# Performance work log

Measured on AMD Instinct MI355X. Metric: run time of the kernel, lower is better.

Reference implementation:

```python
import jax, jax.numpy as jnp
import numpy as np


def lstm_cell(x, h, c, Wih, Whh, bih, bhh):
    # PyTorch LSTM gate order: i, f, g, o
    gates = x @ Wih.T + h @ Whh.T + bih + bhh
    i, f, g, o = jnp.split(gates, 4, axis=-1)
    c_new = jax.nn.sigmoid(f) * c + jax.nn.sigmoid(i) * jnp.tanh(g)
    h_new = jax.nn.sigmoid(o) * jnp.tanh(c_new)
    return h_new, c_new


def setup_inputs() -> dict:
    V, E, H, L, S, B, T = 100000, 256, 256, 2, 256, 16, 128
    G = 4 * H
    s = 0.1  # weight scale to keep activations/gradients well-conditioned
    key = jax.random.key(0)
    ks = jax.random.split(key, 16)
    return {
        'source': jax.random.randint(ks[0], (S, B), 0, V),
        'target_size': T,
        'target_embeddings': jax.random.normal(ks[1], (T, 1, E), dtype=jnp.float32),
        'h0': jax.random.normal(ks[2], (L, B, H), dtype=jnp.float32) * s,
        'c0': jax.random.normal(ks[3], (L, B, H), dtype=jnp.float32) * s,
        'embed_table': jax.random.normal(ks[4], (V, E), dtype=jnp.float32) * s,
        'enc_Wih': jax.random.normal(ks[5], (L, G, E), dtype=jnp.float32) * s,
        'enc_Whh': jax.random.normal(ks[6], (L, G, H), dtype=jnp.float32) * s,
        'enc_bih': jax.random.normal(ks[7], (L, G), dtype=jnp.float32) * s,
        'enc_bhh': jax.random.normal(ks[8], (L, G), dtype=jnp.float32) * s,
        'dec_Wih': jax.random.normal(ks[9], (L, G, E), dtype=jnp.float32) * s,
        'dec_Whh': jax.random.normal(ks[10], (L, G, H), dtype=jnp.float32) * s,
        'dec_bih': jax.random.normal(ks[11], (L, G), dtype=jnp.float32) * s,
        'dec_bhh': jax.random.normal(ks[12], (L, G), dtype=jnp.float32) * s,
        'attn_W': jax.random.normal(ks[13], (1, 2 * H), dtype=jnp.float32) * s,
        'attn_b': jnp.zeros((1,), dtype=jnp.float32),
        'comb_W': jax.random.normal(ks[14], (H, 2 * H), dtype=jnp.float32) * s,
        'comb_b': jnp.zeros((H,), dtype=jnp.float32),
    }


def reference(source, target_size, target_embeddings, h0, c0, embed_table,
              enc_Wih, enc_Whh, enc_bih, enc_bhh,
              dec_Wih, dec_Whh, dec_bih, dec_bhh,
              attn_W, attn_b, comb_W, comb_b):
    L = h0.shape[0]
    B = source.shape[1]

    # ---------------- encoder (per-step LSTM loop -> layer-wise scans) ----
    x = embed_table[source]  # [S, B, E]  (dropout is identity at eval)
    h_fin = []
    for l in range(L):
        def step(carry, xt, l=l):
            h, c = carry
            h, c = lstm_cell(xt, h, c, enc_Wih[l], enc_Whh[l], enc_bih[l], enc_bhh[l])
            return (h, c), h
        (hL, cL), x = jax.lax.scan(step, (h0[l], c0[l]), x)
        h_fin.append(hL)
    hidden_final = jnp.stack(h_fin)   # [L, B, H] == hiddens[-1] in the source
    enc_outputs = x                   # [S, B, H] last-layer hidden per step
    S = enc_outputs.shape[0]

    # NOTE (faithful to source bugs): seq2seq sets both decoder hidden AND
    # cell from encoder_hidden[-1], and the decoder runs its LSTM on the raw
    # input `embedding`, discarding the attention-combined output.
    x0 = jnp.tile(target_embeddings[0, 0], (B, 1))  # [B, E]

    def dec_step(carry, _):
        x, h, c = carry
        # per-step Bahdanau-style attention: computed but UNUSED, as in source
        cat = jnp.concatenate([jnp.broadcast_to(x, (S,) + x.shape), enc_outputs], axis=-1)
        w = jax.nn.softmax(cat @ attn_W.T + attn_b, axis=0)       # [S, B, 1]
        applied = (w * enc_outputs).sum(0)                         # [B, H]
        _combined = jax.nn.relu(jnp.concatenate([x, applied], axis=-1) @ comb_W.T + comb_b)
        # actual recurrence: multi-layer LSTM on the raw input x
        inp = x
        hs, cs = [], []
        for l in range(h.shape[0]):
            hl, cl = lstm_cell(inp, h[l], c[l], dec_Wih[l], dec_Whh[l], dec_bih[l], dec_bhh[l])
            hs.append(hl)
            cs.append(cl)
            inp = hl
        return (inp, jnp.stack(hs), jnp.stack(cs)), inp

    _, ys = jax.lax.scan(dec_step, (x0, hidden_final, hidden_final), None,
                         length=target_size - 1)  # ys: [T-1, B, H]
    H = ys.shape[-1]
    preds = jnp.zeros((target_size, 1, B, H), ys.dtype)
    preds = preds.at[1:].set(ys[:, None])  # predictions[0] stays zero
    return preds
```

## Files before the change

kernel.cpp:

```cpp
#include <hip/hip_runtime.h>
#include <hip/hip_bf16.h>

typedef __attribute__((ext_vector_type(8))) short short8;
typedef __attribute__((ext_vector_type(4))) float f32x4;

#define SEQ   256
#define BB    16
#define EE    256
#define HH    256
#define GG    1024
#define TT    128
#define NWG   32
#define KP    264
#define SLOT_S 8192
#define SENT  0xFF80FF80u
#define MAXTRY (1 << 20)

__device__ __forceinline__ float sigm(float x) { return 1.0f / (1.0f + __expf(-x)); }
__device__ __forceinline__ float tanh_f(float x) {
    float e = __expf(2.0f * x);
    return 1.0f - 2.0f / (e + 1.0f);
}
__device__ __forceinline__ void split2s(float v, short* hi, short* lo) {
    __hip_bfloat16 h = __float2bfloat16(v);
    __hip_bfloat16 l = __float2bfloat16(v - __bfloat162float(h));
    *hi = *(short*)&h; *lo = *(short*)&l;
}
__device__ __forceinline__ f32x4 MFMA(short8 a, short8 b, f32x4 c) {
    return __builtin_amdgcn_mfma_f32_16x16x32_bf16(a, b, c, 0, 0, 0);
}

__device__ __forceinline__ short8 ld16s(const short* p) {
    short8 r;
    asm volatile("global_load_dwordx4 %0, %1, off sc0 sc1" : "=v"(r) : "v"(p));
    return r;
}
__device__ __forceinline__ void st4s(int* p, int v) {
    asm volatile("global_store_dword %0, %1, off sc0 sc1" :: "v"(p), "v"(v) : "memory");
}
__device__ __forceinline__ void vmwait() {
    asm volatile("s_waitcnt vmcnt(0)" ::: "memory");
    __builtin_amdgcn_sched_barrier(0);
}
__device__ __forceinline__ void sync_lds() {
    __builtin_amdgcn_sched_barrier(0);
    asm volatile("s_waitcnt lgkmcnt(0)" ::: "memory");
    __builtin_amdgcn_s_barrier();
    __builtin_amdgcn_sched_barrier(0);
}
union U8 { short8 s; unsigned u[4]; };
__device__ __forceinline__ unsigned chk(short8 f) {
    U8 x; x.s = f;
    return (unsigned)((x.u[0] == SENT) | (x.u[1] == SENT) | (x.u[2] == SENT) | (x.u[3] == SENT));
}

__global__ void k_sent(unsigned* p) {
    long i = ((long)blockIdx.x * 256 + threadIdx.x) * 4;
    p[i] = SENT; p[i + 1] = SENT; p[i + 2] = SENT; p[i + 3] = SENT;
}

__global__ void k_cvt4(const float* __restrict__ s0, const float* __restrict__ s1,
                       const float* __restrict__ s2, const float* __restrict__ s3,
                       char* __restrict__ ws) {
    int g = blockIdx.x >> 11;
    int i = (blockIdx.x & 2047) * 256 + threadIdx.x;
    const float* s = (g == 0) ? s0 : (g == 1) ? s1 : (g == 2) ? s2 : s3;
    __hip_bfloat16* hi = (__hip_bfloat16*)(ws + ((size_t)2 * g) * (1u << 20));
    __hip_bfloat16* lo = (__hip_bfloat16*)(ws + ((size_t)2 * g + 1) * (1u << 20));
    short a, b; split2s(s[i], &a, &b);
    hi[i] = *(__hip_bfloat16*)&a; lo[i] = *(__hip_bfloat16*)&b;
}

__global__ void k_embed(const int* __restrict__ src, const float* __restrict__ tab,
                        __hip_bfloat16* __restrict__ xhi, __hip_bfloat16* __restrict__ xlo) {
    int r = blockIdx.x;
    int j = threadIdx.x;
    long idx = src[r];
    short a, b; split2s(tab[idx * EE + j], &a, &b);
    xhi[(long)r * EE + j] = *(__hip_bfloat16*)&a;
    xlo[(long)r * EE + j] = *(__hip_bfloat16*)&b;
}

__global__ void __launch_bounds__(256) k_gemm_in(
        const __hip_bfloat16* __restrict__ Xhi, const __hip_bfloat16* __restrict__ Xlo,
        const __hip_bfloat16* __restrict__ Whi, const __hip_bfloat16* __restrict__ Wlo,
        const float* __restrict__ bih, const float* __restrict__ bhh,
        float* __restrict__ gates) {
    int lane = threadIdx.x & 63, w = threadIdx.x >> 6;
    int m0 = (blockIdx.x >> 4) * 16;
    int n0 = ((blockIdx.x & 15) * 4 + w) * 16;
    int cc = lane & 15, g = lane >> 4;
    int koff = g * 8;
    const short* xh = (const short*)Xhi + (long)(m0 + cc) * EE + koff;
    const short* xl = (const short*)Xlo + (long)(m0 + cc) * EE + koff;
    const short* wh = (const short*)Whi + (long)(n0 + cc) * EE + koff;
    const short* wl = (const short*)Wlo + (long)(n0 + cc) * EE + koff;
    f32x4 acc1 = {0.f, 0.f, 0.f, 0.f}, acc2 = {0.f, 0.f, 0.f, 0.f};
#pragma unroll
    for (int k = 0; k < EE; k += 32) {
        short8 ah = *(const short8*)(xh + k), al = *(const short8*)(xl + k);
        short8 bh = *(const short8*)(wh + k), bl = *(const short8*)(wl + k);
        acc1 = MFMA(ah, bh, acc1);
        acc2 = MFMA(ah, bl, acc2);
        acc2 = MFMA(al, bh, acc2);
    }
    f32x4 acc = acc1 + acc2;
    int ncol = n0 + cc;
    float bias = bih[ncol] + bhh[ncol];
    int jj = ncol & 255, qq = ncol >> 8;
    int mrow = m0 + g * 4;
#pragma unroll
    for (int r = 0; r < 4; ++r)
        gates[(long)(mrow + r) * GG + jj * 4 + qq] = acc[r] + bias;
}

__device__ __forceinline__ void load_wslice(const short* __restrict__ Wg, int j0,
                                            short* __restrict__ Wl) {
    int tid = threadIdx.x;
    int lr = tid >> 3;
    int q = lr >> 3, jl = lr & 7;
    const short* src = Wg + (long)(q * 256 + j0 + jl) * 256;
    short* dst = Wl + lr * KP;
#pragma unroll
    for (int s = 0; s < 4; ++s) {
        int c = (tid & 7) * 8 + s * 64;
        *(short8*)(dst + c) = *(const short8*)(src + c);
    }
}


__global__ void __launch_bounds__(256, 1) k_enc_coop(
        const float* __restrict__ gates0,
        const short* __restrict__ Whh0h, const short* __restrict__ Whh0l,
        const short* __restrict__ Wih1h, const short* __restrict__ Wih1l,
        const short* __restrict__ Whh1h, const short* __restrict__ Whh1l,
        const float* __restrict__ bih1, const float* __restrict__ bhh1,
        const float* __restrict__ h0p, const float* __restrict__ c0p,
        short* __restrict__ H0, short* __restrict__ H1,
        float* __restrict__ hfin) {
    __shared__ short Wl[6][32 * KP];
    __shared__ float gacc[2][8][16][17];

    int tid = threadIdx.x, bid = blockIdx.x;
    int j0 = bid * 8;
    load_wslice(Whh0h, j0, Wl[0]); load_wslice(Whh0l, j0, Wl[1]);
    load_wslice(Wih1h, j0, Wl[2]); load_wslice(Wih1l, j0, Wl[3]);
    load_wslice(Whh1h, j0, Wl[4]); load_wslice(Whh1l, j0, Wl[5]);

    int bb = (tid & 127) >> 3, jl = tid & 7, j = j0 + jl, lay = tid >> 7;
    float creg = c0p[lay * 4096 + bb * 256 + j];
    float bs[4] = {0.f, 0.f, 0.f, 0.f};
    if (lay) {
#pragma unroll
        for (int q = 0; q < 4; ++q) bs[q] = bih1[q * 256 + j] + bhh1[q * 256 + j];
    }
    f32x4 gnew = {0.f, 0.f, 0.f, 0.f};
    if (!lay) {
        gnew = *(const f32x4*)(gates0 + ((long)bb * 256 + j) * 4);
    }
    {
        float hv = h0p[lay * 4096 + bb * 256 + j];
        short sh, sl; split2s(hv, &sh, &sl);
        int mh = (unsigned short)sh, ml = (unsigned short)sl;
        int nh = __shfl_down(mh, 1), nl = __shfl_down(ml, 1);
        int* dst = (int*)(lay ? H1 : H0);
        if (!(jl & 1)) {
            int idx = bb * 256 + bid * 8 + (jl >> 1);
            st4s(dst + idx, mh | (nh << 16));
            st4s(dst + idx + 4, ml | (nl << 16));
        }
    }

    int lane = tid & 63, w = tid >> 6, cc = lane & 15, g4 = lane >> 4;
    int tw = w & 1, kb = (w >> 1) * 128;
    int abase = cc * 512 + kb * 2 + g4 * 16;
    int wr = (tw * 16 + cc) * KP + kb + (g4 * 8);

    for (int i = 0; i <= SEQ; ++i) {
        bool actL0 = (i < SEQ), actL1 = (i >= 1);
        int par = i & 1;

        short8 f0h[4], f0l[4], f1h[4], f1l[4];
        const short* b0 = H0 + (long)i * SLOT_S + abase;
        const short* b1 = H1 + (long)(i - 1) * SLOT_S + abase;
        int tries = 0;
        while (true) {
#pragma unroll
            for (int ki = 0; ki < 4; ++ki) {
                f0h[ki] = ld16s(b0 + ki * 64);
                f0l[ki] = ld16s(b0 + ki * 64 + 8);
            }
            if (actL1) {
#pragma unroll
                for (int ki = 0; ki < 4; ++ki) {
                    f1h[ki] = ld16s(b1 + ki * 64);
                    f1l[ki] = ld16s(b1 + ki * 64 + 8);
                }
            }
            vmwait();
            unsigned bad = 0;
#pragma unroll
            for (int ki = 0; ki < 4; ++ki) bad |= chk(f0h[ki]) | chk(f0l[ki]);
            if (actL1) {
#pragma unroll
                for (int ki = 0; ki < 4; ++ki) bad |= chk(f1h[ki]) | chk(f1l[ki]);
            }
            if (!__any((int)bad) || ++tries > MAXTRY) break;
        }

        float gpre[4] = {0.f, 0.f, 0.f, 0.f};
        if (!lay) {
#pragma unroll
            for (int q = 0; q < 4; ++q) gpre[q] = gnew[q];
            if (i + 1 < SEQ)
                gnew = *(const f32x4*)(gates0 + ((long)((i + 1) * BB + bb) * 256 + j) * 4);
        }

        f32x4 z = {0.f, 0.f, 0.f, 0.f};
        f32x4 s0 = z, s1 = z;
        if (actL0) {
            f32x4 a1 = z, a2 = z;
#pragma unroll
            for (int ki = 0; ki < 4; ++ki) {
                short8 wh  = *(const short8*)(Wl[0] + wr + ki * 32);
                short8 wl2 = *(const short8*)(Wl[1] + wr + ki * 32);
                a1 = MFMA(f0h[ki], wh, a1);
                a2 = MFMA(f0h[ki], wl2, a2);
                a2 = MFMA(f0l[ki], wh, a2);
            }
            s0 = a1 + a2;
        }
        if (actL1) {
            f32x4 a1 = z, a2 = z;
#pragma unroll
            for (int ki = 0; ki < 4; ++ki) {
                a1 = MFMA(f0h[ki], *(const short8*)(Wl[2] + wr + ki * 32), a1);
                a2 = MFMA(f0h[ki], *(const short8*)(Wl[3] + wr + ki * 32), a2);
                a2 = MFMA(f0l[ki], *(const short8*)(Wl[2] + wr + ki * 32), a2);
                a1 = MFMA(f1h[ki], *(const short8*)(Wl[4] + wr + ki * 32), a1);
                a2 = MFMA(f1h[ki], *(const short8*)(Wl[5] + wr + ki * 32), a2);
                a2 = MFMA(f1l[ki], *(const short8*)(Wl[4] + wr + ki * 32), a2);
            }
            s1 = a1 + a2;
        }
#pragma unroll
        for (int r = 0; r < 4; ++r) {
            gacc[par][w][g4 * 4 + r][cc] = s0[r];
            gacc[par][4 + w][g4 * 4 + r][cc] = s1[r];
        }
        sync_lds();

        bool act = lay ? actL1 : actL0;
        if (act) {
            int t = lay ? (i - 1) : i;
            float gv[4];
#pragma unroll
            for (int q = 0; q < 4; ++q) {
                int lr = q * 8 + jl, tl = lr >> 4, c = lr & 15;
                gv[q] = lay ? (gacc[par][4 + tl][bb][c] + gacc[par][6 + tl][bb][c] + bs[q])
                            : (gacc[par][tl][bb][c] + gacc[par][2 + tl][bb][c] + gpre[q]);
            }
            float c = sigm(gv[1]) * creg + sigm(gv[0]) * tanh_f(gv[2]);
            creg = c;
            float h = sigm(gv[3]) * tanh_f(c);
            short sh, sl; split2s(h, &sh, &sl);
            int mh = (unsigned short)sh, ml = (unsigned short)sl;
            int nh = __shfl_down(mh, 1), nl = __shfl_down(ml, 1);
            int* dst = (int*)(lay ? (H1 + (long)i * SLOT_S) : (H0 + (long)(i + 1) * SLOT_S));
            if (!(jl & 1)) {
                int idx = bb * 256 + bid * 8 + (jl >> 1);
                st4s(dst + idx, mh | (nh << 16));
                st4s(dst + idx + 4, ml | (nl << 16));
            }
            if (t == SEQ - 1) hfin[lay * 4096 + bb * 256 + j] = h;
        }
    }
}

__global__ void __launch_bounds__(256, 1) k_dec_coop(
        const short* __restrict__ Wihh, const short* __restrict__ Wihl,
        const short* __restrict__ Whhh, const short* __restrict__ Whhl,
        const float* __restrict__ dbih, const float* __restrict__ dbhh,
        const float* __restrict__ tef, const float* __restrict__ hfin,
        short* __restrict__ H0, short* __restrict__ H1,
        short* __restrict__ TE,
        float* __restrict__ preds) {
    __shared__ short Wl[8][32 * KP];
    __shared__ float gacc[2][4][16][17];
    const int WN = GG * EE;

    int tid = threadIdx.x, bid = blockIdx.x;
    int j0 = bid * 8;
    load_wslice(Wihh, j0, Wl[0]);      load_wslice(Wihl, j0, Wl[1]);
    load_wslice(Whhh, j0, Wl[2]);      load_wslice(Whhl, j0, Wl[3]);
    load_wslice(Wihh + WN, j0, Wl[4]); load_wslice(Wihl + WN, j0, Wl[5]);
    load_wslice(Whhh + WN, j0, Wl[6]); load_wslice(Whhl + WN, j0, Wl[7]);

    int bb = (tid & 127) >> 3, jl = tid & 7, j = j0 + jl;
    float c0r = 0.f, c1r = 0.f;
    float bs0[4] = {0,0,0,0}, bs1[4] = {0,0,0,0};
    if (tid < 128) {
        float h0v = hfin[bb * 256 + j], h1v = hfin[4096 + bb * 256 + j];
        c0r = h0v; c1r = h1v;
        preds[bb * 256 + j] = 0.0f;
        int idx = bb * 256 + bid * 8 + (jl >> 1);
        short sh, sl;
        split2s(tef[j], &sh, &sl);
        {
            int mh = (unsigned short)sh, ml = (unsigned short)sl;
            int nh = __shfl_down(mh, 1), nl = __shfl_down(ml, 1);
            if (!(jl & 1)) { st4s((int*)TE + idx, mh | (nh << 16));
                             st4s((int*)TE + idx + 4, ml | (nl << 16)); }
        }
        split2s(h0v, &sh, &sl);
        {
            int mh = (unsigned short)sh, ml = (unsigned short)sl;
            int nh = __shfl_down(mh, 1), nl = __shfl_down(ml, 1);
            if (!(jl & 1)) { st4s((int*)H0 + idx, mh | (nh << 16));
                             st4s((int*)H0 + idx + 4, ml | (nl << 16)); }
        }
        split2s(h1v, &sh, &sl);
        {
            int mh = (unsigned short)sh, ml = (unsigned short)sl;
            int nh = __shfl_down(mh, 1), nl = __shfl_down(ml, 1);
            if (!(jl & 1)) { st4s((int*)H1 + idx, mh | (nh << 16));
                             st4s((int*)H1 + idx + 4, ml | (nl << 16)); }
        }
#pragma unroll
        for (int q = 0; q < 4; ++q) {
            bs0[q] = dbih[q*256+j] + dbhh[q*256+j];
            bs1[q] = dbih[GG + q*256+j] + dbhh[GG + q*256+j];
        }
    }

    int lane = tid & 63, w = tid >> 6, cc = lane & 15, g4 = lane >> 4;
    int tw = w & 1, kb = (w >> 1) * 128;
    int abase = cc * 512 + kb * 2 + g4 * 16;
    int wr = (tw * 16 + cc) * KP + kb + (g4 * 8);

    short8 xAh[4], xAl[4], xBh[4], xBl[4], h1ih[4], h1il[4];

    {
        const short* p0 = H0 + abase;
        const short* p1 = H1 + abase;
        int tries = 0;
        while (true) {
#pragma unroll
            for (int ki = 0; ki < 4; ++ki) {
                xBh[ki] = ld16s(p0 + ki * 64); xBl[ki] = ld16s(p0 + ki * 64 + 8);
                h1ih[ki] = ld16s(p1 + ki * 64); h1il[ki] = ld16s(p1 + ki * 64 + 8);
            }
            vmwait();
            unsigned bad = 0;
#pragma unroll
            for (int ki = 0; ki < 4; ++ki)
                bad |= chk(xBh[ki]) | chk(xBl[ki]) | chk(h1ih[ki]) | chk(h1il[ki]);
            if (!__any((int)bad) || ++tries > MAXTRY) break;
        }
    }

    for (int t = 0; t < TT - 1; ++t) {
        {
            const short* px = (t ? H1 + (long)t * SLOT_S : TE) + abase;
            int tries = 0;
            while (true) {
#pragma unroll
                for (int ki = 0; ki < 4; ++ki) {
                    xAh[ki] = ld16s(px + ki * 64); xAl[ki] = ld16s(px + ki * 64 + 8);
                }
                vmwait();
                unsigned bad = 0;
#pragma unroll
                for (int ki = 0; ki < 4; ++ki) bad |= chk(xAh[ki]) | chk(xAl[ki]);
                if (!__any((int)bad) || ++tries > MAXTRY) break;
            }
            f32x4 a1 = {0.f,0.f,0.f,0.f}, a2 = {0.f,0.f,0.f,0.f};
#pragma unroll
            for (int ki = 0; ki < 4; ++ki) {
                a1 = MFMA(xAh[ki], *(const short8*)(Wl[0] + wr + ki * 32), a1);
                a2 = MFMA(xAh[ki], *(const short8*)(Wl[1] + wr + ki * 32), a2);
                a2 = MFMA(xAl[ki], *(const short8*)(Wl[0] + wr + ki * 32), a2);
                a1 = MFMA(xBh[ki], *(const short8*)(Wl[2] + wr + ki * 32), a1);
                a2 = MFMA(xBh[ki], *(const short8*)(Wl[3] + wr + ki * 32), a2);
                a2 = MFMA(xBl[ki], *(const short8*)(Wl[2] + wr + ki * 32), a2);
            }
            f32x4 accs = a1 + a2;
#pragma unroll
            for (int r = 0; r < 4; ++r) gacc[0][w][g4 * 4 + r][cc] = accs[r];
        }
        sync_lds();
        if (tid < 128) {
            float gv[4];
#pragma unroll
            for (int q = 0; q < 4; ++q) {
                int lr = q * 8 + jl;
                gv[q] = gacc[0][lr >> 4][bb][lr & 15] + gacc[0][2 + (lr >> 4)][bb][lr & 15] + bs0[q];
            }
            float c = sigm(gv[1]) * c0r + sigm(gv[0]) * tanh_f(gv[2]);
            c0r = c;
            float h = sigm(gv[3]) * tanh_f(c);
            short sh, sl; split2s(h, &sh, &sl);
            int mh = (unsigned short)sh, ml = (unsigned short)sl;
            int nh = __shfl_down(mh, 1), nl = __shfl_down(ml, 1);
            if (!(jl & 1)) {
                int idx = bb * 256 + bid * 8 + (jl >> 1);
                int* dst = (int*)(H0 + (long)(t + 1) * SLOT_S);
                st4s(dst + idx, mh | (nh << 16));
                st4s(dst + idx + 4, ml | (nl << 16));
            }
        }
        {
            const short* px = H0 + (long)(t + 1) * SLOT_S + abase;
            int tries = 0;
            while (true) {
#pragma unroll
                for (int ki = 0; ki < 4; ++ki) {
                    xBh[ki] = ld16s(px + ki * 64); xBl[ki] = ld16s(px + ki * 64 + 8);
                }
                vmwait();
                unsigned bad = 0;
#pragma unroll
                for (int ki = 0; ki < 4; ++ki) bad |= chk(xBh[ki]) | chk(xBl[ki]);
                if (!__any((int)bad) || ++tries > MAXTRY) break;
            }
            f32x4 a1 = {0.f,0.f,0.f,0.f}, a2 = {0.f,0.f,0.f,0.f};
#pragma unroll
            for (int ki = 0; ki < 4; ++ki) {
                short8 hh = t ? xAh[ki] : h1ih[ki];
                short8 hl = t ? xAl[ki] : h1il[ki];
                a1 = MFMA(xBh[ki], *(const short8*)(Wl[4] + wr + ki * 32), a1);
                a2 = MFMA(xBh[ki], *(const short8*)(Wl[5] + wr + ki * 32), a2);
                a2 = MFMA(xBl[ki], *(const short8*)(Wl[4] + wr + ki * 32), a2);
                a1 = MFMA(hh, *(const short8*)(Wl[6] + wr + ki * 32), a1);
                a2 = MFMA(hh, *(const short8*)(Wl[7] + wr + ki * 32), a2);
                a2 = MFMA(hl, *(const short8*)(Wl[6] + wr + ki * 32), a2);
            }
            f32x4 accs = a1 + a2;
#pragma unroll
            for (int r = 0; r < 4; ++r) gacc[1][w][g4 * 4 + r][cc] = accs[r];
        }
        sync_lds();
        if (tid < 128) {
            float gv[4];
#pragma unroll
            for (int q = 0; q < 4; ++q) {
                int lr = q * 8 + jl;
                gv[q] = gacc[1][lr >> 4][bb][lr & 15] + gacc[1][2 + (lr >> 4)][bb][lr & 15] + bs1[q];
            }
            float c = sigm(gv[1]) * c1r + sigm(gv[0]) * tanh_f(gv[2]);
            c1r = c;
            float h = sigm(gv[3]) * tanh_f(c);
            short sh, sl; split2s(h, &sh, &sl);
            int mh = (unsigned short)sh, ml = (unsigned short)sl;
            int nh = __shfl_down(mh, 1), nl = __shfl_down(ml, 1);
            if (!(jl & 1)) {
                int idx = bb * 256 + bid * 8 + (jl >> 1);
                int* dst = (int*)(H1 + (long)(t + 1) * SLOT_S);
                st4s(dst + idx, mh | (nh << 16));
                st4s(dst + idx + 4, ml | (nl << 16));
            }
            preds[((long)(t + 1) * BB + bb) * HH + j] = h;
        }
    }
}

extern "C" void kernel_launch(void* const* d_in, const int* in_sizes, int n_in,
                              void* d_out, int out_size, void* d_ws, size_t ws_size,
                              hipStream_t stream) {
    const int*   src   = (const int*)  d_in[0];
    const float* te    = (const float*)d_in[2];
    const float* h0    = (const float*)d_in[3];
    const float* c0    = (const float*)d_in[4];
    const float* table = (const float*)d_in[5];
    const float* eWih  = (const float*)d_in[6];
    const float* eWhh  = (const float*)d_in[7];
    const float* ebih  = (const float*)d_in[8];
    const float* ebhh  = (const float*)d_in[9];
    const float* dWih  = (const float*)d_in[10];
    const float* dWhh  = (const float*)d_in[11];
    const float* dbih  = (const float*)d_in[12];
    const float* dbhh  = (const float*)d_in[13];
    float* preds = (float*)d_out;

    const int WN = GG * EE;
    const size_t MB = 1u << 20;
    char* ws = (char*)d_ws;
    short* eWih_hi = (short*)(ws + 0 * MB);
    short* eWih_lo = (short*)(ws + 1 * MB);
    short* eWhh_hi = (short*)(ws + 2 * MB);
    short* eWhh_lo = (short*)(ws + 3 * MB);
    short* dWih_hi = (short*)(ws + 4 * MB);
    short* dWih_lo = (short*)(ws + 5 * MB);
    short* dWhh_hi = (short*)(ws + 6 * MB);
    short* dWhh_lo = (short*)(ws + 7 * MB);
    short* Xa_hi   = (short*)(ws + 8 * MB);
    short* Xa_lo   = (short*)(ws + 10 * MB);
    float* hfin    = (float*)(ws + 12 * MB);
    short* slots   = (short*)(ws + 13 * MB);
    short* SLe0 = slots;
    short* SLe1 = SLe0 + (long)257 * SLOT_S;
    short* SLd0 = SLe1 + (long)257 * SLOT_S;
    short* SLd1 = SLd0 + (long)128 * SLOT_S;
    short* SLte = SLd1 + (long)128 * SLOT_S;
    float* gates0 = (float*)(ws + 26 * MB);

    k_sent<<<3084, 256, 0, stream>>>((unsigned*)slots);

    k_cvt4<<<8192, 256, 0, stream>>>(eWih, eWhh, dWih, dWhh, ws);

    k_embed<<<4096, 256, 0, stream>>>(src, table, (__hip_bfloat16*)Xa_hi, (__hip_bfloat16*)Xa_lo);
    k_gemm_in<<<4096, 256, 0, stream>>>((__hip_bfloat16*)Xa_hi, (__hip_bfloat16*)Xa_lo,
                                        (__hip_bfloat16*)eWih_hi, (__hip_bfloat16*)eWih_lo,
                                        ebih, ebhh, gates0);
    k_enc_coop<<<NWG, 256, 0, stream>>>(gates0, eWhh_hi, eWhh_lo,
                                        eWih_hi + WN, eWih_lo + WN, eWhh_hi + WN, eWhh_lo + WN,
                                        ebih + GG, ebhh + GG, h0, c0,
                                        SLe0, SLe1, hfin);

    k_dec_coop<<<NWG, 256, 0, stream>>>(dWih_hi, dWih_lo, dWhh_hi, dWhh_lo,
                                        dbih, dbhh, te, hfin,
                                        SLd0, SLd1, SLte, preds);
    (void)in_sizes; (void)n_in; (void)out_size; (void)ws_size;
}
```

Measured before the change: 2.369 ms.

## Add per-workgroup ready flags to gate cross-block polling of hidden-state slots

Adds per-step, per-workgroup flag arrays. Each block publishes a flag after writing its slice of h, and one wave polls the 32 small flags before the block reads the full hidden-state slots. Before this, every thread repeatedly reloaded whole bf16 slot fragments and checked them for sentinels. The goal is cheaper spinning with less memory traffic during the wait. The cost is an extra __syncthreads plus flag store and poll per step, and the gates0 prefetch moves to the end of each iteration.

```diff
diff --git a/kernel.cpp b/kernel.cpp
--- a/kernel.cpp
+++ b/kernel.cpp
@@ -33,6 +33,12 @@
 __device__ __forceinline__ short8 ld16s(const short* p) {
     short8 r;
     asm volatile("global_load_dwordx4 %0, %1, off sc0 sc1" : "=v"(r) : "v"(p));
+    return r;
+}
+__device__ __forceinline__ int ld4f(const int* p) {
+    int r;
+    asm volatile("global_load_dword %0, %1, off sc0 sc1\n\ts_waitcnt vmcnt(0)"
+                 : "=v"(r) : "v"(p) : "memory");
     return r;
 }
 __device__ __forceinline__ void st4s(int* p, int v) {
@@ -137,7 +143,8 @@
         const float* __restrict__ bih1, const float* __restrict__ bhh1,
         const float* __restrict__ h0p, const float* __restrict__ c0p,
         short* __restrict__ H0, short* __restrict__ H1,
-        float* __restrict__ hfin) {
+        float* __restrict__ hfin,
+        int* __restrict__ FE0, int* __restrict__ FE1) {
     __shared__ short Wl[6][32 * KP];
     __shared__ float gacc[2][8][16][17];
 
@@ -170,6 +177,8 @@
             st4s(dst + idx + 4, ml | (nl << 16));
         }
     }
+    __syncthreads();
+    if (tid == 0) { st4s(FE0 + bid, 1); st4s(FE1 + bid, 1); }
 
     int lane = tid & 63, w = tid >> 6, cc = lane & 15, g4 = lane >> 4;
     int tw = w & 1, kb = (w >> 1) * 128;
@@ -179,6 +188,19 @@
     for (int i = 0; i <= SEQ; ++i) {
         bool actL0 = (i < SEQ), actL1 = (i >= 1);
         int par = i & 1;
+
+        if (tid >= 192) {
+            int ln = tid - 192;
+            const int* fp = (ln < 32) ? (FE0 + (long)i * 32 + ln)
+                                      : (FE1 + (long)(i - 1) * 32 + (ln - 32));
+            bool active = (ln < 32) ? true : actL1;
+            int tries = 0;
+            while (true) {
+                int v = active ? ld4f(fp) : 1;
+                if (__all(v != (int)SENT) || ++tries > MAXTRY) break;
+            }
+        }
+        sync_lds();
 
         short8 f0h[4], f0l[4], f1h[4], f1l[4];
         const short* b0 = H0 + (long)i * SLOT_S + abase;
@@ -212,8 +234,6 @@
         if (!lay) {
 #pragma unroll
             for (int q = 0; q < 4; ++q) gpre[q] = gnew[q];
-            if (i + 1 < SEQ)
-                gnew = *(const f32x4*)(gates0 + ((long)((i + 1) * BB + bb) * 256 + j) * 4);
         }
 
         f32x4 z = {0.f, 0.f, 0.f, 0.f};
@@ -274,6 +294,14 @@
             }
             if (t == SEQ - 1) hfin[lay * 4096 + bb * 256 + j] = h;
         }
+
+        __syncthreads();
+        if (tid == 0) {
+            if (actL0) st4s(FE0 + (long)(i + 1) * 32 + bid, 1);
+            if (actL1) st4s(FE1 + (long)i * 32 + bid, 1);
+        }
+        if (!lay && i + 1 < SEQ)
+            gnew = *(const f32x4*)(gates0 + ((long)((i + 1) * BB + bb) * 256 + j) * 4);
     }
 }
 
@@ -284,7 +312,8 @@
         const float* __restrict__ tef, const float* __restrict__ hfin,
         short* __restrict__ H0, short* __restrict__ H1,
         short* __restrict__ TE,
-        float* __restrict__ preds) {
+        float* __restrict__ preds,
+        int* __restrict__ FD0, int* __restrict__ FD1, int* __restrict__ FT) {
     __shared__ short Wl[8][32 * KP];
     __shared__ float gacc[2][4][16][17];
     const int WN = GG * EE;
@@ -332,6 +361,8 @@
             bs1[q] = dbih[GG + q*256+j] + dbhh[GG + q*256+j];
         }
     }
+    __syncthreads();
+    if (tid == 0) { st4s(FT + bid, 1); st4s(FD0 + bid, 1); st4s(FD1 + bid, 1); }
 
     int lane = tid & 63, w = tid >> 6, cc = lane & 15, g4 = lane >> 4;
     int tw = w & 1, kb = (w >> 1) * 128;
@@ -341,6 +372,16 @@
     short8 xAh[4], xAl[4], xBh[4], xBl[4], h1ih[4], h1il[4];
 
     {
+        if (tid >= 192) {
+            int ln = tid - 192;
+            const int* fp = (ln < 32) ? (FD0 + ln) : (FD1 + (ln - 32));
+            int tries = 0;
+            while (true) {
+                int v = ld4f(fp);
+                if (__all(v != (int)SENT) || ++tries > MAXTRY) break;
+            }
+        }
+        sync_lds();
         const short* p0 = H0 + abase;
         const short* p1 = H1 + abase;
         int tries = 0;
@@ -361,6 +402,16 @@
 
     for (int t = 0; t < TT - 1; ++t) {
         {
+            if (tid >= 192) {
+                int ln = tid - 192;
+                const int* fp = t ? (FD1 + (long)t * 32 + ln) : (FT + ln);
+                int tries = 0;
+                while (true) {
+                    int v = (ln < 32) ? ld4f(fp) : 1;
+                    if (__all(v != (int)SENT) || ++tries > MAXTRY) break;
+                }
+            }
+            sync_lds();
             const short* px = (t ? H1 + (long)t * SLOT_S : TE) + abase;
             int tries = 0;
             while (true) {
@@ -409,7 +460,20 @@
                 st4s(dst + idx + 4, ml | (nl << 16));
             }
         }
+        __syncthreads();
+        if (tid == 0) st4s(FD0 + (long)(t + 1) * 32 + bid, 1);
+
         {
+            if (tid >= 192) {
+                int ln = tid - 192;
+                const int* fp = FD0 + (long)(t + 1) * 32 + ln;
+                int tries = 0;
+                while (true) {
+                    int v = (ln < 32) ? ld4f(fp) : 1;
+                    if (__all(v != (int)SENT) || ++tries > MAXTRY) break;
+                }
+            }
+            sync_lds();
             const short* px = H0 + (long)(t + 1) * SLOT_S + abase;
             int tries = 0;
             while (true) {
@@ -461,6 +525,8 @@
             }
             preds[((long)(t + 1) * BB + bb) * HH + j] = h;
         }
+        __syncthreads();
+        if (tid == 0) st4s(FD1 + (long)(t + 1) * 32 + bid, 1);
     }
 }
 
@@ -502,9 +568,15 @@
     short* SLd0 = SLe1 + (long)257 * SLOT_S;
     short* SLd1 = SLd0 + (long)128 * SLOT_S;
     short* SLte = SLd1 + (long)128 * SLOT_S;
+    int*   FL   = (int*)(SLte + (long)1 * SLOT_S);
+    int* FE0 = FL;
+    int* FE1 = FL + 257 * 32;
+    int* FD0 = FE1 + 257 * 32;
+    int* FD1 = FD0 + 128 * 32;
+    int* FT  = FD1 + 128 * 32;
     float* gates0 = (float*)(ws + 26 * MB);
 
-    k_sent<<<3084, 256, 0, stream>>>((unsigned*)slots);
+    k_sent<<<3109, 256, 0, stream>>>((unsigned*)slots);
 
     k_cvt4<<<8192, 256, 0, stream>>>(eWih, eWhh, dWih, dWhh, ws);
 
@@ -515,10 +587,10 @@
     k_enc_coop<<<NWG, 256, 0, stream>>>(gates0, eWhh_hi, eWhh_lo,
                                         eWih_hi + WN, eWih_lo + WN, eWhh_hi + WN, eWhh_lo + WN,
                                         ebih + GG, ebhh + GG, h0, c0,
-                                        SLe0, SLe1, hfin);
+                                        SLe0, SLe1, hfin, FE0, FE1);
 
     k_dec_coop<<<NWG, 256, 0, stream>>>(dWih_hi, dWih_lo, dWhh_hi, dWhh_lo,
                                         dbih, dbhh, te, hfin,
-                                        SLd0, SLd1, SLte, preds);
+                                        SLd0, SLd1, SLte, preds, FD0, FD1, FT);
     (void)in_sizes; (void)n_in; (void)out_size; (void)ws_size;
 }
```

Result: faster. 2.122 ms, median of 2 (-10.4%).
